# Optimization experiments

Hardware: AMD Instinct MI355X
Metric: run time of the kernel (lower is better)

The kernel has to match this reference:

```python
import jax, jax.numpy as jnp
import numpy as np

B, T, D, I, C, H = 8192, 128, 7, 128, 10, 64
L = 2 ** D
SUBSET = int(I * 0.8)  # feature_subset_size = 102


def setup_inputs() -> dict:
    key = jax.random.key(0)
    ks = jax.random.split(key, 7)
    x = jax.random.normal(ks[0], (B, I), dtype=jnp.float32)
    # exact feature-subset mask: SUBSET ones per (tree, depth) row
    r = jax.random.uniform(ks[1], (T, D, I))
    ranks = jnp.argsort(jnp.argsort(r, axis=-1), axis=-1)
    feature_mask = (ranks < SUBSET).astype(jnp.float32)
    thresholds = jax.random.normal(ks[2], (T, D), dtype=jnp.float32)
    leaf_outputs = jax.random.normal(ks[3], (T, L, C), dtype=jnp.float32)
    W1 = jax.random.normal(ks[4], (I, H), dtype=jnp.float32) * 0.08
    b1 = jnp.zeros((H,), dtype=jnp.float32)
    W2 = jax.random.normal(ks[5], (H, T), dtype=jnp.float32) * 0.12
    b2 = jnp.zeros((T,), dtype=jnp.float32)
    return {"x": x, "feature_mask": feature_mask, "thresholds": thresholds,
            "leaf_outputs": leaf_outputs, "W1": W1, "b1": b1, "W2": W2, "b2": b2}


def reference(x, feature_mask, thresholds, leaf_outputs, W1, b1, W2, b2):
    depth = thresholds.shape[1]
    # split logits: masked feature sum minus threshold, per (batch, tree, depth)
    z = jnp.einsum('bi,tdi->btd', x, feature_mask) - thresholds[None, :, :]
    s = 0.5 * (z / (1.0 + jnp.abs(z)) + 1.0)  # scaled softsign split in (0,1)
    # probabilistic path routing: doubling concat, identical to torch loop
    p = jnp.ones((x.shape[0], feature_mask.shape[0], 1), dtype=x.dtype)
    for d in range(depth):
        sd = s[:, :, d:d + 1]            # [B, T, 1]
        p = jnp.concatenate([p * sd, p * (1.0 - sd)], axis=-1)  # [B, T, 2^(d+1)]
    leaf_probs = jax.nn.softmax(leaf_outputs, axis=-1)           # [T, L, C]
    tree_outputs = jnp.einsum('btl,tlc->btc', p, leaf_probs)     # [B, T, C]
    # instance-wise attention over trees (eval mode: no dropout)
    attn = jax.nn.softmax(jax.nn.relu(x @ W1 + b1) @ W2 + b2, axis=-1)  # [B, T]
    return jnp.sum(tree_outputs * attn[:, :, None], axis=1)     # [B, C]
```

## Files before the change

kernel.cpp:

```cpp
#include <hip/hip_runtime.h>
#include <hip/hip_bf16.h>
#include <hip/hip_fp16.h>


#define BB 8192
#define TT 128
#define II 128
#define CC 10
#define HH 64

#define OFF_LPB 524288

typedef __attribute__((ext_vector_type(8))) short short8;
typedef __attribute__((ext_vector_type(16))) float floatx16;

static __device__ inline unsigned int pkbf(float lo, float hi) {
  __hip_bfloat162 h = __float22bfloat162_rn(make_float2(lo, hi));
  unsigned int u;
  __builtin_memcpy(&u, &h, 4);
  return u;
}

static __device__ inline unsigned int pkh(float lo, float hi) {
  __half2 h = __float22half2_rn(make_float2(lo, hi));
  unsigned int u;
  __builtin_memcpy(&u, &h, 4);
  return u;
}

static __device__ inline short8 cvt8(float4 a, float4 b) {
  union { short8 v; unsigned int u[4]; } r;
  r.u[0] = pkbf(a.x, a.y);
  r.u[1] = pkbf(a.z, a.w);
  r.u[2] = pkbf(b.x, b.y);
  r.u[3] = pkbf(b.z, b.w);
  return r.v;
}

__global__ __launch_bounds__(256, 2) void prep_kernel(
    const float* __restrict__ x, const float* __restrict__ lo,
    const float* __restrict__ W1, const float* __restrict__ b1,
    const float* __restrict__ W2, const float* __restrict__ b2,
    __half* __restrict__ attnB, unsigned int* __restrict__ lpbG) {
  __shared__ __align__(16) char smem_raw[18432];
  const int blk = blockIdx.x;
  const int tid = threadIdx.x;
  const int wv = tid >> 6, lane = tid & 63;
  const int half = lane >> 5, l31 = lane & 31;

  if (blk < 64) {
    const int b0 = blk * 128 + wv * 32;

    short8 axf[8];
    const float* xrow = x + (size_t)(b0 + l31) * II + half * 8;
#pragma unroll
    for (int s = 0; s < 8; ++s)
      axf[s] = cvt8(*(const float4*)(xrow + s * 16),
                    *(const float4*)(xrow + s * 16 + 4));

    floatx16 acch[2];
#pragma unroll
    for (int i = 0; i < 16; ++i) { acch[0][i] = 0.f; acch[1][i] = 0.f; }
#pragma unroll
    for (int s = 0; s < 8; ++s) {
#pragma unroll
      for (int tile = 0; tile < 2; ++tile) {
        union { short8 v; unsigned int u[4]; } wf;
#pragma unroll
        for (int jp = 0; jp < 4; ++jp) {
          int k0 = s * 16 + half * 8 + jp * 2;
          float f0 = W1[(size_t)k0 * HH + tile * 32 + l31];
          float f1 = W1[(size_t)(k0 + 1) * HH + tile * 32 + l31];
          wf.u[jp] = pkbf(f0, f1);
        }
        acch[tile] = __builtin_amdgcn_mfma_f32_32x32x16_bf16(
            axf[s], wf.v, acch[tile], 0, 0, 0);
      }
    }
    __hip_bfloat16* hids = (__hip_bfloat16*)smem_raw + wv * (32 * 72);
#pragma unroll
    for (int tile = 0; tile < 2; ++tile) {
      float bh = b1[tile * 32 + l31];
#pragma unroll
      for (int r = 0; r < 16; ++r) {
        int row = (r & 3) + 8 * (r >> 2) + 4 * half;
        hids[row * 72 + tile * 32 + l31] =
            __float2bfloat16(fmaxf(acch[tile][r] + bh, 0.f));
      }
    }
    __syncthreads();

    short8 ahf[4];
#pragma unroll
    for (int s = 0; s < 4; ++s)
      ahf[s] = *(const short8*)(hids + l31 * 72 + s * 16 + half * 8);

    floatx16 accl[4];
#pragma unroll
    for (int tile = 0; tile < 4; ++tile) {
#pragma unroll
      for (int i = 0; i < 16; ++i) accl[tile][i] = 0.f;
#pragma unroll
      for (int s = 0; s < 4; ++s) {
        union { short8 v; unsigned int u[4]; } wf;
#pragma unroll
        for (int jp = 0; jp < 4; ++jp) {
          int k0 = s * 16 + half * 8 + jp * 2;
          float f0 = W2[(size_t)k0 * TT + tile * 32 + l31];
          float f1 = W2[(size_t)(k0 + 1) * TT + tile * 32 + l31];
          wf.u[jp] = pkbf(f0, f1);
        }
        accl[tile] = __builtin_amdgcn_mfma_f32_32x32x16_bf16(
            ahf[s], wf.v, accl[tile], 0, 0, 0);
      }
      float bt = b2[tile * 32 + l31];
#pragma unroll
      for (int i = 0; i < 16; ++i) accl[tile][i] += bt;
    }

    float mrow[16];
#pragma unroll
    for (int r = 0; r < 16; ++r)
      mrow[r] = fmaxf(fmaxf(accl[0][r], accl[1][r]),
                      fmaxf(accl[2][r], accl[3][r]));
#pragma unroll
    for (int msk = 1; msk <= 16; msk <<= 1)
#pragma unroll
      for (int r = 0; r < 16; ++r)
        mrow[r] = fmaxf(mrow[r], __shfl_xor(mrow[r], msk, 64));
    float srow[16];
#pragma unroll
    for (int r = 0; r < 16; ++r) srow[r] = 0.f;
#pragma unroll
    for (int tile = 0; tile < 4; ++tile)
#pragma unroll
      for (int r = 0; r < 16; ++r) {
        float e = __expf(accl[tile][r] - mrow[r]);
        accl[tile][r] = e;
        srow[r] += e;
      }
#pragma unroll
    for (int msk = 1; msk <= 16; msk <<= 1)
#pragma unroll
      for (int r = 0; r < 16; ++r)
        srow[r] += __shfl_xor(srow[r], msk, 64);
#pragma unroll
    for (int r = 0; r < 16; ++r) srow[r] = 1.f / srow[r];

#pragma unroll
    for (int tile = 0; tile < 4; ++tile)
#pragma unroll
      for (int r = 0; r < 16; ++r) {
        int row = (r & 3) + 8 * (r >> 2) + 4 * half;
        attnB[(size_t)(b0 + row) * TT + tile * 32 + l31] =
            __float2half(accl[tile][r] * srow[r]);
      }

  } else {
    float* lps = (float*)smem_raw;
    const int t0 = (blk - 64) * 2;
    {
      int tl = tid >> 7, l = tid & 127;
      const float* row = lo + ((size_t)(t0 + tl) * 128 + l) * CC;
      float v[CC];
      float m = -1e30f;
#pragma unroll
      for (int c = 0; c < CC; ++c) { v[c] = row[c]; m = fmaxf(m, v[c]); }
      float s = 0.f;
#pragma unroll
      for (int c = 0; c < CC; ++c) { v[c] = __expf(v[c] - m); s += v[c]; }
      float inv = 1.f / s;
      float* o = lps + (tl * 128 + l) * 12;
#pragma unroll
      for (int c = 0; c < CC; ++c) o[c] = v[c] * inv;
    }
    __syncthreads();

#pragma unroll
    for (int jj = 0; jj < 2; ++jj) {
      int idx = jj * 256 + tid;
      if (idx < 320) {
        int tl = idx / 160, rem = idx - tl * 160;
        int s = rem / 20, e = rem - s * 20;
        int n = e >> 1, hf = e & 1;
        unsigned int wd[4];
#pragma unroll
        for (int jp = 0; jp < 4; ++jp) {
          int l0 = s * 16 + hf * 8 + jp * 2;
          float f0 = lps[(tl * 128 + l0) * 12 + n];
          float f1 = lps[(tl * 128 + l0 + 1) * 12 + n];
          wd[jp] = pkh(f0, f1);
        }
        ((uint4*)lpbG)[(size_t)(t0 + tl) * 160 + s * 20 + n * 2 + hf] =
            make_uint4(wd[0], wd[1], wd[2], wd[3]);
      }
    }
  }
}

__global__ __launch_bounds__(256, 4) void main_kernel(
    const float* __restrict__ x, const float* __restrict__ mask,
    const float* __restrict__ thr, const __half* __restrict__ attnB,
    const unsigned int* __restrict__ lpbG, float* __restrict__ out) {
  __shared__ __align__(16) char smem_raw[38912];
  const int tid = threadIdx.x;
  const int wv = tid >> 6, lane = tid & 63;
  const int half = lane >> 5, l31 = lane & 31;
  const int bg2 = blockIdx.x >> 4;
  const int tg = blockIdx.x & 15;

  __half* zsl = (__half*)smem_raw;
  uint4* attnV4 = (uint4*)(smem_raw + 16384);
  uint4* lpB4 = (uint4*)(smem_raw + 18432);

  if (tid < 128)
    attnV4[tid] = ((const uint4*)attnB)[(size_t)(bg2 * 128 + tid) * 16 + tg];
  {
    const uint4* lg = (const uint4*)lpbG + (size_t)tg * 1280;
#pragma unroll
    for (int j = 0; j < 5; ++j) lpB4[j * 256 + tid] = lg[j * 256 + tid];
  }

  {
    const int m0 = tg * 56;
    short8 xf[8];
    const float* xrow = x + (size_t)(bg2 * 128 + wv * 32 + l31) * II + half * 8;
#pragma unroll
    for (int s = 0; s < 8; ++s)
      xf[s] = cvt8(*(const float4*)(xrow + s * 16),
                   *(const float4*)(xrow + s * 16 + 4));

#pragma unroll
    for (int tile = 0; tile < 2; ++tile) {
      int mr = m0 + tile * 28 + l31; if (mr > 895) mr = 895;
      const float* mrow = mask + (size_t)mr * II + half * 8;
      short8 af[8];
#pragma unroll
      for (int s = 0; s < 8; ++s)
        af[s] = cvt8(*(const float4*)(mrow + s * 16),
                     *(const float4*)(mrow + s * 16 + 4));
      floatx16 acc;
#pragma unroll
      for (int i = 0; i < 16; ++i) acc[i] = 0.f;
#pragma unroll
      for (int s = 0; s < 8; ++s)
        acc = __builtin_amdgcn_mfma_f32_32x32x16_bf16(af[s], xf[s], acc, 0, 0, 0);

#pragma unroll
      for (int r = 0; r < 16; ++r) {
        int row = (r & 3) + 8 * (r >> 2) + 4 * half;
        if (row < 28) {
          int mrr = m0 + tile * 28 + row;
          float th = thr[mrr > 895 ? 895 : mrr];
          int tl = row / 7;
          int d = row - tl * 7;
          float z = acc[r] - th;
          float o = 0.5f * (z / (1.f + fabsf(z)) + 1.f);
          zsl[((tl + tile * 4) * 128 + wv * 32 + l31) * 8 + d] = __float2half(o);
        }
      }
    }
  }
  __syncthreads();

  {
    const uint4* zsl4 = (const uint4*)smem_raw;
    const int bl = wv * 32 + l31;

    __half av[8];
    *(uint4*)av = attnV4[bl];

    floatx16 acc;
#pragma unroll
    for (int i = 0; i < 16; ++i) acc[i] = 0.f;

#pragma unroll
    for (int it = 0; it < 8; ++it) {
      uint4 sv = zsl4[it * 128 + bl];
      uint4 bf[8];
#pragma unroll
      for (int s = 0; s < 8; ++s)
        bf[s] = (l31 < CC) ? lpB4[(it * 8 + s) * 20 + l31 * 2 + half]
                           : make_uint4(0u, 0u, 0u, 0u);

      const __half* sh = (const __half*)&sv;
      float s0 = __half2float(sh[0]), s1 = __half2float(sh[1]);
      float s2 = __half2float(sh[2]), s3 = __half2float(sh[3]);
      float s4 = __half2float(sh[4]), s5 = __half2float(sh[5]);
      float s6 = __half2float(sh[6]);
      float A  = __half2float(av[it]);

      float s0c = 1.f - s0, s1c = 1.f - s1, s2c = 1.f - s2;
      float t0 = s0 * s1, t1 = s0c * s1, t2 = s0 * s1c, t3 = s0c * s1c;
      float pl[8];
      pl[0] = t0 * s2;  pl[1] = t1 * s2;  pl[2] = t2 * s2;  pl[3] = t3 * s2;
      pl[4] = t0 * s2c; pl[5] = t1 * s2c; pl[6] = t2 * s2c; pl[7] = t3 * s2c;
      float sel3 = half ? (1.f - s3) : s3;
      float Af = A * sel3;
      float s4c = 1.f - s4, s5c = 1.f - s5;
      float as6 = Af * s6, as6c = Af * (1.f - s6);
      float u0 = s4 * s5, u1 = s4c * s5, u2 = s4 * s5c, u3 = s4c * s5c;
      float wv8[8];
      wv8[0] = u0 * as6;  wv8[1] = u1 * as6;
      wv8[2] = u2 * as6;  wv8[3] = u3 * as6;
      wv8[4] = u0 * as6c; wv8[5] = u1 * as6c;
      wv8[6] = u2 * as6c; wv8[7] = u3 * as6c;
      __half2 pl2[4];
#pragma unroll
      for (int jp = 0; jp < 4; ++jp)
        pl2[jp] = __float22half2_rn(make_float2(pl[jp * 2], pl[jp * 2 + 1]));

#pragma unroll
      for (int s = 0; s < 8; ++s) {
        union { short8 v; __half2 h[4]; } a0;
        __half2 w2 = __half2half2(__float2half(wv8[s]));
#pragma unroll
        for (int jp = 0; jp < 4; ++jp) a0.h[jp] = __hmul2(pl2[jp], w2);
        acc = __builtin_amdgcn_mfma_f32_32x32x16_f16(
            a0.v, *(const short8*)&bf[s], acc, 0, 0, 0);
      }
    }

    __syncthreads();
    float* red = (float*)(smem_raw + 18432);
    if (l31 < CC) {
#pragma unroll
      for (int r = 0; r < 16; ++r) {
        int row = (r & 3) + 8 * (r >> 2) + 4 * half;
        red[(wv * 32 + row) * 10 + l31] = acc[r];
      }
    }
    __syncthreads();
#pragma unroll
    for (int j = 0; j < 5; ++j) {
      int idx = tid + 256 * j;
      atomicAdd(out + (size_t)bg2 * 1280 + idx, red[idx]);
    }
  }
}

extern "C" void kernel_launch(void* const* d_in, const int* in_sizes, int n_in,
                              void* d_out, int out_size, void* d_ws, size_t ws_size,
                              hipStream_t stream) {
  const float* x    = (const float*)d_in[0];
  const float* mask = (const float*)d_in[1];
  const float* thr  = (const float*)d_in[2];
  const float* lo   = (const float*)d_in[3];
  const float* W1   = (const float*)d_in[4];
  const float* b1   = (const float*)d_in[5];
  const float* W2   = (const float*)d_in[6];
  const float* b2   = (const float*)d_in[7];
  float* out = (float*)d_out;
  float* ws  = (float*)d_ws;

  __half*       attnB = (__half*)ws;
  unsigned int* LPb   = (unsigned int*)(ws + OFF_LPB);

  hipMemsetAsync(out, 0, (size_t)out_size * sizeof(float), stream);
  prep_kernel<<<128, 256, 0, stream>>>(x, lo, W1, b1, W2, b2, attnB, LPb);
  main_kernel<<<1024, 256, 0, stream>>>(x, mask, thr, attnB, LPb, out);
}
```

Before: 117.4 us.

## Pre-convert inputs to bf16 in prep, drop LDS staging, raise occupancy

The prep kernel now converts x and the feature mask to bf16 in workspace and zeroes the output, replacing the separate memset. The main kernel reads bf16 operands directly, loads attention weights and leaf tables from global memory instead of staging them in shared memory, and hoists threshold loads. Shared memory shrinks, which allows raising launch bounds to 6 blocks per CU, and block indices are remapped to group tree tiles for cache reuse. The cost is an extra conversion pass in prep and more global/L2 traffic for the leaf tables.

```diff
diff --git a/kernel.cpp b/kernel.cpp
--- a/kernel.cpp
+++ b/kernel.cpp
@@ -10,6 +10,8 @@
 #define HH 64
 
 #define OFF_LPB 524288
+#define OFF_XBF 606208
+#define OFF_MBF 1130496
 
 typedef __attribute__((ext_vector_type(8))) short short8;
 typedef __attribute__((ext_vector_type(16))) float floatx16;
@@ -38,10 +40,13 @@
 }
 
 __global__ __launch_bounds__(256, 2) void prep_kernel(
-    const float* __restrict__ x, const float* __restrict__ lo,
+    const float* __restrict__ x, const float* __restrict__ mask,
+    const float* __restrict__ lo,
     const float* __restrict__ W1, const float* __restrict__ b1,
     const float* __restrict__ W2, const float* __restrict__ b2,
-    __half* __restrict__ attnB, unsigned int* __restrict__ lpbG) {
+    __half* __restrict__ attnB, unsigned int* __restrict__ lpbG,
+    unsigned short* __restrict__ xbf, unsigned short* __restrict__ mbf,
+    float* __restrict__ out) {
   __shared__ __align__(16) char smem_raw[18432];
   const int blk = blockIdx.x;
   const int tid = threadIdx.x;
@@ -156,7 +161,7 @@
             __float2half(accl[tile][r] * srow[r]);
       }
 
-  } else {
+  } else if (blk < 128) {
     float* lps = (float*)smem_raw;
     const int t0 = (blk - 64) * 2;
     {
@@ -195,50 +200,63 @@
             make_uint4(wd[0], wd[1], wd[2], wd[3]);
       }
     }
+  } else if (blk < 199) {
+    const float* src;
+    unsigned short* dst;
+    size_t base;
+    if (blk < 192) { src = x;    dst = xbf; base = (size_t)(blk - 128) * 16384; }
+    else           { src = mask; dst = mbf; base = (size_t)(blk - 192) * 16384; }
+#pragma unroll
+    for (int j = 0; j < 8; ++j) {
+      size_t e = base + (size_t)j * 2048 + (size_t)tid * 8;
+      float4 a = *(const float4*)(src + e);
+      float4 b = *(const float4*)(src + e + 4);
+      *(short8*)(dst + e) = cvt8(a, b);
+    }
+  } else {
+    ((float4*)out)[(blk - 199) * 256 + tid] = make_float4(0.f, 0.f, 0.f, 0.f);
   }
 }
 
-__global__ __launch_bounds__(256, 4) void main_kernel(
-    const float* __restrict__ x, const float* __restrict__ mask,
+__global__ __launch_bounds__(256, 6) void main_kernel(
+    const unsigned short* __restrict__ xbf, const unsigned short* __restrict__ mbf,
     const float* __restrict__ thr, const __half* __restrict__ attnB,
     const unsigned int* __restrict__ lpbG, float* __restrict__ out) {
-  __shared__ __align__(16) char smem_raw[38912];
+  __shared__ __align__(16) char smem_raw[16384];
   const int tid = threadIdx.x;
   const int wv = tid >> 6, lane = tid & 63;
   const int half = lane >> 5, l31 = lane & 31;
-  const int bg2 = blockIdx.x >> 4;
-  const int tg = blockIdx.x & 15;
+  const int phys = blockIdx.x;
+  const int bg2 = (phys & 7) + ((phys >> 7) << 3);
+  const int tg  = (phys >> 3) & 15;
+  const int bl = wv * 32 + l31;
 
   __half* zsl = (__half*)smem_raw;
-  uint4* attnV4 = (uint4*)(smem_raw + 16384);
-  uint4* lpB4 = (uint4*)(smem_raw + 18432);
-
-  if (tid < 128)
-    attnV4[tid] = ((const uint4*)attnB)[(size_t)(bg2 * 128 + tid) * 16 + tg];
-  {
-    const uint4* lg = (const uint4*)lpbG + (size_t)tg * 1280;
-#pragma unroll
-    for (int j = 0; j < 5; ++j) lpB4[j * 256 + tid] = lg[j * 256 + tid];
-  }
+
+  __half av[8];
+  *(uint4*)av = ((const uint4*)attnB)[(size_t)(bg2 * 128 + bl) * 16 + tg];
 
   {
     const int m0 = tg * 56;
     short8 xf[8];
-    const float* xrow = x + (size_t)(bg2 * 128 + wv * 32 + l31) * II + half * 8;
-#pragma unroll
-    for (int s = 0; s < 8; ++s)
-      xf[s] = cvt8(*(const float4*)(xrow + s * 16),
-                   *(const float4*)(xrow + s * 16 + 4));
+    const unsigned short* xr = xbf + (size_t)(bg2 * 128 + bl) * II + half * 8;
+#pragma unroll
+    for (int s = 0; s < 8; ++s) xf[s] = *(const short8*)(xr + s * 16);
 
 #pragma unroll
     for (int tile = 0; tile < 2; ++tile) {
       int mr = m0 + tile * 28 + l31; if (mr > 895) mr = 895;
-      const float* mrow = mask + (size_t)mr * II + half * 8;
+      const unsigned short* mrow = mbf + (size_t)mr * II + half * 8;
       short8 af[8];
 #pragma unroll
-      for (int s = 0; s < 8; ++s)
-        af[s] = cvt8(*(const float4*)(mrow + s * 16),
-                     *(const float4*)(mrow + s * 16 + 4));
+      for (int s = 0; s < 8; ++s) af[s] = *(const short8*)(mrow + s * 16);
+      float th[16];
+#pragma unroll
+      for (int r = 0; r < 16; ++r) {
+        int row = (r & 3) + 8 * (r >> 2) + 4 * half;
+        int mrr = m0 + tile * 28 + row;
+        th[r] = thr[mrr > 895 ? 895 : mrr];
+      }
       floatx16 acc;
 #pragma unroll
       for (int i = 0; i < 16; ++i) acc[i] = 0.f;
@@ -250,25 +268,19 @@
       for (int r = 0; r < 16; ++r) {
         int row = (r & 3) + 8 * (r >> 2) + 4 * half;
         if (row < 28) {
-          int mrr = m0 + tile * 28 + row;
-          float th = thr[mrr > 895 ? 895 : mrr];
           int tl = row / 7;
           int d = row - tl * 7;
-          float z = acc[r] - th;
+          float z = acc[r] - th[r];
           float o = 0.5f * (z / (1.f + fabsf(z)) + 1.f);
-          zsl[((tl + tile * 4) * 128 + wv * 32 + l31) * 8 + d] = __float2half(o);
+          zsl[((tl + tile * 4) * 128 + bl) * 8 + d] = __float2half(o);
         }
       }
     }
   }
-  __syncthreads();
 
   {
     const uint4* zsl4 = (const uint4*)smem_raw;
-    const int bl = wv * 32 + l31;
-
-    __half av[8];
-    *(uint4*)av = attnV4[bl];
+    const uint4* lpt = (const uint4*)lpbG + (size_t)tg * 1280;
 
     floatx16 acc;
 #pragma unroll
@@ -276,12 +288,12 @@
 
 #pragma unroll
     for (int it = 0; it < 8; ++it) {
+      uint4 bf[8];
+#pragma unroll
+      for (int s = 0; s < 8; ++s)
+        bf[s] = (l31 < CC) ? lpt[(it * 8 + s) * 20 + l31 * 2 + half]
+                           : make_uint4(0u, 0u, 0u, 0u);
       uint4 sv = zsl4[it * 128 + bl];
-      uint4 bf[8];
-#pragma unroll
-      for (int s = 0; s < 8; ++s)
-        bf[s] = (l31 < CC) ? lpB4[(it * 8 + s) * 20 + l31 * 2 + half]
-                           : make_uint4(0u, 0u, 0u, 0u);
 
       const __half* sh = (const __half*)&sv;
       float s0 = __half2float(sh[0]), s1 = __half2float(sh[1]);
@@ -322,7 +334,7 @@
     }
 
     __syncthreads();
-    float* red = (float*)(smem_raw + 18432);
+    float* red = (float*)smem_raw;
     if (l31 < CC) {
 #pragma unroll
       for (int r = 0; r < 16; ++r) {
@@ -353,10 +365,12 @@
   float* out = (float*)d_out;
   float* ws  = (float*)d_ws;
 
-  __half*       attnB = (__half*)ws;
-  unsigned int* LPb   = (unsigned int*)(ws + OFF_LPB);
-
-  hipMemsetAsync(out, 0, (size_t)out_size * sizeof(float), stream);
-  prep_kernel<<<128, 256, 0, stream>>>(x, lo, W1, b1, W2, b2, attnB, LPb);
-  main_kernel<<<1024, 256, 0, stream>>>(x, mask, thr, attnB, LPb, out);
-}
+  __half*        attnB = (__half*)ws;
+  unsigned int*  LPb   = (unsigned int*)(ws + OFF_LPB);
+  unsigned short* xbf  = (unsigned short*)(ws + OFF_XBF);
+  unsigned short* mbf  = (unsigned short*)(ws + OFF_MBF);
+
+  prep_kernel<<<279, 256, 0, stream>>>(x, mask, lo, W1, b1, W2, b2,
+                                       attnB, LPb, xbf, mbf, out);
+  main_kernel<<<1024, 256, 0, stream>>>(xbf, mbf, thr, attnB, LPb, out);
+}
```

After: 104.7 us. 1.12x faster.
